# Performance work log

Measured on AMD Instinct MI355X. Metric: run time of the kernel, lower is better.

The kernel has to match this reference:

```python
import jax, jax.numpy as jnp
import numpy as np

BATCH, HID, STEPS = 64, 2048, 30

def setup_inputs() -> dict:
    key = jax.random.key(0)
    ks = jax.random.split(key, 7)
    s = 1.0 / np.sqrt(HID)  # pytorch LSTM/Linear init scale
    return {
        "monthly_token": jax.random.normal(ks[0], (BATCH, HID), jnp.float32),
        "steps": STEPS,
        "W_ih": jax.random.uniform(ks[1], (4 * HID, HID), jnp.float32, -s, s),
        "W_hh": jax.random.uniform(ks[2], (4 * HID, HID), jnp.float32, -s, s),
        "b_ih": jax.random.uniform(ks[3], (4 * HID,), jnp.float32, -s, s),
        "b_hh": jax.random.uniform(ks[4], (4 * HID,), jnp.float32, -s, s),
        "W_out": jax.random.uniform(ks[5], (1, HID), jnp.float32, -s, s),
        "b_out": jax.random.uniform(ks[6], (1,), jnp.float32, -s, s),
    }

def reference(monthly_token, steps, W_ih, W_hh, b_ih, b_hh, W_out, b_out):
    H = monthly_token.shape[1]
    h0 = monthly_token                      # (B, H) initial hidden
    c0 = jnp.zeros_like(h0)
    x0 = jnp.zeros_like(h0)                 # first lstm input is zeros

    def step(carry, _):
        h, c, x = carry
        # PyTorch gate order: input, forget, cell(g), output
        gates = x @ W_ih.T + b_ih + h @ W_hh.T + b_hh   # (B, 4H)
        i, f, g, o = jnp.split(gates, 4, axis=-1)
        i = jax.nn.sigmoid(i)
        f = jax.nn.sigmoid(f)
        g = jnp.tanh(g)
        o = jax.nn.sigmoid(o)
        c_new = f * c + i * g
        h_new = o * jnp.tanh(c_new)
        y = h_new @ W_out.T + b_out          # (B, 1) daily value
        # feedback: next input is the lstm output (= h_new for 1-layer LSTM)
        return (h_new, c_new, h_new), y[:, 0]

    _, ys = jax.lax.scan(step, (h0, c0, x0), xs=None, length=steps)
    return ys.T                               # (B, steps)
```

## Files before the change

kernel.cpp:

```cpp
#include <hip/hip_runtime.h>
#include <cmath>


#define HID   2048
#define BATCH 64
#define G4    8192
#define NCU   256
#define HGRP  (HID * BATCH / 8)
#define NFLAGS 512

typedef __attribute__((ext_vector_type(8))) _Float16 half8;
typedef __attribute__((ext_vector_type(4))) float f32x4;

#define LDS_BYTES 155648

__global__ void k_init(const float* __restrict__ token, const float* __restrict__ bih,
                       const float* __restrict__ bhh, half8* __restrict__ h0p,
                       float* __restrict__ bsum, unsigned* __restrict__ flags) {
    int g = blockIdx.x * 256 + threadIdx.x;
    int l = g & 63, nt = (g >> 6) & 3, kt = g >> 8;
    int n = nt * 16 + (l & 15);
    int k0 = kt * 32 + (l >> 4) * 8;
    const float4* ps = (const float4*)(token + (size_t)n * HID + k0);
    float4 a = ps[0], b = ps[1];
    half8 v;
    v[0]=(_Float16)a.x; v[1]=(_Float16)a.y; v[2]=(_Float16)a.z; v[3]=(_Float16)a.w;
    v[4]=(_Float16)b.x; v[5]=(_Float16)b.y; v[6]=(_Float16)b.z; v[7]=(_Float16)b.w;
    h0p[g] = v;
    if (g < G4) bsum[g] = bih[g] + bhh[g];
    if (g < NFLAGS) flags[g] = 0u;
}

__global__ __launch_bounds__(512, 2)
void k_lstm(const float* __restrict__ wih, const float* __restrict__ whh,
            const float* __restrict__ bsum, const float* __restrict__ wout,
            _Float16* __restrict__ hbuf,
            float* __restrict__ ypart,
            unsigned* __restrict__ flags, int steps) {
    extern __shared__ char smem[];
    half8* Wlds = (half8*)smem;
    f32x4* red4 = (f32x4*)(smem + 131072);

    const int tid  = threadIdx.x;
    const int blk  = blockIdx.x;
    const int lane = tid & 63;
    const int w    = tid >> 6;
    const int half = w & 1;
    const int ks   = w >> 1;
    const int q    = lane >> 4;
    const int col  = lane & 15;

    for (int idx = tid; idx < 2 * 64 * 64; idx += 512) {
        int l = idx & 63, kt = (idx >> 6) & 63, m2 = idx >> 12;
        int m = l & 15;
        int gate = m2 * 2 + (m >> 3);
        int row  = gate * HID + blk * 8 + (m & 7);
        int colw = kt * 32 + (l >> 4) * 8;
        const float4* p = (const float4*)(whh + (size_t)row * HID + colw);
        float4 a = p[0], b = p[1];
        half8 v;
        v[0]=(_Float16)a.x; v[1]=(_Float16)a.y; v[2]=(_Float16)a.z; v[3]=(_Float16)a.w;
        v[4]=(_Float16)b.x; v[5]=(_Float16)b.y; v[6]=(_Float16)b.z; v[7]=(_Float16)b.w;
        Wlds[idx] = v;
    }

    float biasA[4] = {0,0,0,0}, biasB[4] = {0,0,0,0}, wj4[4] = {0,0,0,0};
    float c4[4] = {0.0f, 0.0f, 0.0f, 0.0f};
    if (w < 2) {
        #pragma unroll
        for (int r = 0; r < 4; ++r) {
            int rA = 4 * q + r;
            int rB = 16 + 4 * q + r;
            biasA[r] = bsum[(rA >> 3) * HID + blk * 8 + (rA & 7)];
            biasB[r] = bsum[(rB >> 3) * HID + blk * 8 + (rB & 7)];
            wj4[r]   = wout[blk * 8 + (q & 1) * 4 + r];
        }
    }
    __syncthreads();

    for (int t = 0; t < steps; ++t) {
        if (t) {
            while (__hip_atomic_load(&flags[half * NCU + ks * 64 + lane],
                                     __ATOMIC_RELAXED, __HIP_MEMORY_SCOPE_AGENT)
                   < (unsigned)t)
                __builtin_amdgcn_s_sleep(1);
            asm volatile("" ::: "memory");
        }
        const half8* hp = (const half8*)(hbuf + (size_t)t * HID * BATCH);
        const int ktb = ks * 16;
        half8 bfr[32];
        #pragma unroll
        for (int kk = 0; kk < 16; ++kk) {
            bfr[2 * kk + 0] = hp[((ktb + kk) * 4 + half * 2 + 0) * 64 + lane];
            bfr[2 * kk + 1] = hp[((ktb + kk) * 4 + half * 2 + 1) * 64 + lane];
        }
        f32x4 a00 = {0,0,0,0}, a01 = {0,0,0,0}, a10 = {0,0,0,0}, a11 = {0,0,0,0};
        #pragma unroll
        for (int kk = 0; kk < 16; ++kk) {
            int kt = ktb + kk;
            half8 av0 = Wlds[(kt) * 64 + lane];
            half8 av1 = Wlds[(64 + kt) * 64 + lane];
            a00 = __builtin_amdgcn_mfma_f32_16x16x32_f16(av0, bfr[2 * kk + 0], a00, 0, 0, 0);
            a01 = __builtin_amdgcn_mfma_f32_16x16x32_f16(av0, bfr[2 * kk + 1], a01, 0, 0, 0);
            a10 = __builtin_amdgcn_mfma_f32_16x16x32_f16(av1, bfr[2 * kk + 0], a10, 0, 0, 0);
            a11 = __builtin_amdgcn_mfma_f32_16x16x32_f16(av1, bfr[2 * kk + 1], a11, 0, 0, 0);
        }
        if (ks == 1 || ks == 3) {
            int srow = (ks == 3 ? 2 : 0) + half;
            red4[(srow * 4 + 0) * 64 + lane] = a00;
            red4[(srow * 4 + 1) * 64 + lane] = a01;
            red4[(srow * 4 + 2) * 64 + lane] = a10;
            red4[(srow * 4 + 3) * 64 + lane] = a11;
        }
        __syncthreads();
        if (ks == 0) {
            int srow = half;
            a00 += red4[(srow * 4 + 0) * 64 + lane];
            a01 += red4[(srow * 4 + 1) * 64 + lane];
            a10 += red4[(srow * 4 + 2) * 64 + lane];
            a11 += red4[(srow * 4 + 3) * 64 + lane];
        } else if (ks == 2) {
            int srow = 2 + half;
            a00 += red4[(srow * 4 + 0) * 64 + lane];
            a01 += red4[(srow * 4 + 1) * 64 + lane];
            a10 += red4[(srow * 4 + 2) * 64 + lane];
            a11 += red4[(srow * 4 + 3) * 64 + lane];
            int sdst = 4 + half;
            red4[(sdst * 4 + 0) * 64 + lane] = a00;
            red4[(sdst * 4 + 1) * 64 + lane] = a01;
            red4[(sdst * 4 + 2) * 64 + lane] = a10;
            red4[(sdst * 4 + 3) * 64 + lane] = a11;
        }
        __syncthreads();
        if (w < 2) {
            int srow = 4 + half;
            a00 += red4[(srow * 4 + 0) * 64 + lane];
            a01 += red4[(srow * 4 + 1) * 64 + lane];
            a10 += red4[(srow * 4 + 2) * 64 + lane];
            a11 += red4[(srow * 4 + 3) * 64 + lane];
            #pragma unroll
            for (int r = 0; r < 4; ++r) {
                a00[r] += biasA[r]; a01[r] += biasA[r];
                a10[r] += biasB[r]; a11[r] += biasB[r];
            }
            float x00[4], x01[4], x10[4], x11[4];
            #pragma unroll
            for (int r = 0; r < 4; ++r) {
                x00[r] = __shfl_xor(a00[r], 32);
                x01[r] = __shfl_xor(a01[r], 32);
                x10[r] = __shfl_xor(a10[r], 32);
                x11[r] = __shfl_xor(a11[r], 32);
            }
            const bool lo = (lane < 32);
            float hv[4];
            #pragma unroll
            for (int r = 0; r < 4; ++r) {
                float gi = lo ? a00[r] : x01[r];
                float gf = lo ? x00[r] : a01[r];
                float gg = lo ? a10[r] : x11[r];
                float go = lo ? x10[r] : a11[r];
                float iv = 1.0f / (1.0f + __expf(-gi));
                float fv = 1.0f / (1.0f + __expf(-gf));
                float eg = __expf(2.0f * gg);
                float gv = 1.0f - 2.0f / (eg + 1.0f);
                float ov = 1.0f / (1.0f + __expf(-go));
                c4[r] = fv * c4[r] + iv * gv;
                float ec = __expf(2.0f * c4[r]);
                float th = 1.0f - 2.0f / (ec + 1.0f);
                hv[r] = ov * th;
            }
            if (t < steps - 1) {
                union { unsigned short us[4]; unsigned long long ull; } pk;
                #pragma unroll
                for (int r = 0; r < 4; ++r) {
                    _Float16 hf = (_Float16)hv[r];
                    pk.us[r] = *(unsigned short*)&hf;
                }
                const int nt = half * 2 + (q >> 1);
                const size_t g = (size_t)((blk >> 2) * 4 + nt) * 64
                               + (blk & 3) * 16 + col;
                unsigned long long* dst = (unsigned long long*)
                    (hbuf + (size_t)(t + 1) * HID * BATCH + g * 8) + (q & 1);
                __hip_atomic_store(dst, pk.ull, __ATOMIC_RELAXED,
                                   __HIP_MEMORY_SCOPE_AGENT);
                asm volatile("s_waitcnt vmcnt(0)" ::: "memory");
                if (lane == 0)
                    __hip_atomic_store(&flags[half * NCU + blk], (unsigned)(t + 1),
                                       __ATOMIC_RELAXED, __HIP_MEMORY_SCOPE_AGENT);
            }
            float yp = wj4[0] * hv[0] + wj4[1] * hv[1]
                     + wj4[2] * hv[2] + wj4[3] * hv[3];
            yp += __shfl_xor(yp, 16);
            if ((q & 1) == 0)
                ypart[((size_t)t * NCU + blk) * 64
                      + half * 32 + (q >> 1) * 16 + col] = yp;
        }
        if (t == 0) {
            for (int idx = tid; idx < 2 * 64 * 64; idx += 512) {
                int l = idx & 63, kt = (idx >> 6) & 63, m2 = idx >> 12;
                int m = l & 15;
                int gate = m2 * 2 + (m >> 3);
                int row  = gate * HID + blk * 8 + (m & 7);
                int colw = kt * 32 + (l >> 4) * 8;
                const float4* p = (const float4*)(wih + (size_t)row * HID + colw);
                float4 a = p[0], b = p[1];
                half8 v = Wlds[idx];
                v[0] = (_Float16)((float)v[0] + a.x); v[1] = (_Float16)((float)v[1] + a.y);
                v[2] = (_Float16)((float)v[2] + a.z); v[3] = (_Float16)((float)v[3] + a.w);
                v[4] = (_Float16)((float)v[4] + b.x); v[5] = (_Float16)((float)v[5] + b.y);
                v[6] = (_Float16)((float)v[6] + b.z); v[7] = (_Float16)((float)v[7] + b.w);
                Wlds[idx] = v;
            }
            __syncthreads();
        }
    }
}

__global__ __launch_bounds__(512)
void k_yout(const float* __restrict__ ypart, const float* __restrict__ bout,
            float* __restrict__ out, int steps) {
    __shared__ float red[8][64];
    int t = blockIdx.x;
    int tid = threadIdx.x;
    int b = tid & 63, ch = tid >> 6;
    const float* p = ypart + (size_t)t * NCU * 64 + b;
    float s = 0.0f;
    #pragma unroll 8
    for (int cu = ch * 32; cu < ch * 32 + 32; ++cu) s += p[(size_t)cu * 64];
    red[ch][b] = s;
    __syncthreads();
    if (tid < 64) {
        float r = bout[0];
        #pragma unroll
        for (int u = 0; u < 8; ++u) r += red[u][tid];
        out[(size_t)tid * steps + t] = r;
    }
}

extern "C" void kernel_launch(void* const* d_in, const int* in_sizes, int n_in,
                              void* d_out, int out_size, void* d_ws, size_t ws_size,
                              hipStream_t stream) {
    const float* token = (const float*)d_in[0];
    const float* wih   = (const float*)d_in[2];
    const float* whh   = (const float*)d_in[3];
    const float* bih   = (const float*)d_in[4];
    const float* bhh   = (const float*)d_in[5];
    const float* wout  = (const float*)d_in[6];
    const float* bout  = (const float*)d_in[7];
    float* out = (float*)d_out;
    const int steps = out_size / BATCH;

    char* ws = (char*)d_ws;
    size_t off = 0;
    auto carve = [&](size_t bytes) -> void* {
        void* p = ws + off;
        off = (off + bytes + 255) & ~(size_t)255;
        return p;
    };
    _Float16* hbuf  = (_Float16*)carve((size_t)(steps + 1) * HID * BATCH * 2);
    float*    bsum  = (float*)carve((size_t)G4 * 4);
    float*    ypart = (float*)carve((size_t)steps * NCU * 64 * 4);
    unsigned* flags = (unsigned*)carve(NFLAGS * 4);

    hipFuncSetAttribute(reinterpret_cast<const void*>(&k_lstm),
                        hipFuncAttributeMaxDynamicSharedMemorySize, LDS_BYTES);

    k_init<<<dim3(HGRP / 256), dim3(256), 0, stream>>>(
        token, bih, bhh, (half8*)hbuf, bsum, flags);

    k_lstm<<<dim3(NCU), dim3(512), LDS_BYTES, stream>>>(
        wih, whh, bsum, wout, hbuf, ypart, flags, steps);

    k_yout<<<dim3(steps), dim3(512), 0, stream>>>(ypart, bout, out, steps);
}
```

Baseline: 440.6 us.

## Replace per-step flag barrier with sentinel-valued hidden-state polling

```diff
diff --git a/kernel.cpp b/kernel.cpp
--- a/kernel.cpp
+++ b/kernel.cpp
@@ -7,7 +7,7 @@
 #define G4    8192
 #define NCU   256
 #define HGRP  (HID * BATCH / 8)
-#define NFLAGS 512
+#define SENT  0xFFFFFFFFFFFFFFFFull
 
 typedef __attribute__((ext_vector_type(8))) _Float16 half8;
 typedef __attribute__((ext_vector_type(4))) float f32x4;
@@ -15,20 +15,26 @@
 #define LDS_BYTES 155648
 
 __global__ void k_init(const float* __restrict__ token, const float* __restrict__ bih,
-                       const float* __restrict__ bhh, half8* __restrict__ h0p,
-                       float* __restrict__ bsum, unsigned* __restrict__ flags) {
-    int g = blockIdx.x * 256 + threadIdx.x;
-    int l = g & 63, nt = (g >> 6) & 3, kt = g >> 8;
-    int n = nt * 16 + (l & 15);
-    int k0 = kt * 32 + (l >> 4) * 8;
-    const float4* ps = (const float4*)(token + (size_t)n * HID + k0);
-    float4 a = ps[0], b = ps[1];
-    half8 v;
-    v[0]=(_Float16)a.x; v[1]=(_Float16)a.y; v[2]=(_Float16)a.z; v[3]=(_Float16)a.w;
-    v[4]=(_Float16)b.x; v[5]=(_Float16)b.y; v[6]=(_Float16)b.z; v[7]=(_Float16)b.w;
-    h0p[g] = v;
-    if (g < G4) bsum[g] = bih[g] + bhh[g];
-    if (g < NFLAGS) flags[g] = 0u;
+                       const float* __restrict__ bhh, half8* __restrict__ hbuf8,
+                       float* __restrict__ bsum) {
+    int slot = blockIdx.x >> 6;
+    int g = (blockIdx.x & 63) * 256 + threadIdx.x;
+    if (slot == 0) {
+        int l = g & 63, nt = (g >> 6) & 3, kt = g >> 8;
+        int n = nt * 16 + (l & 15);
+        int k0 = kt * 32 + (l >> 4) * 8;
+        const float4* ps = (const float4*)(token + (size_t)n * HID + k0);
+        float4 a = ps[0], b = ps[1];
+        half8 v;
+        v[0]=(_Float16)a.x; v[1]=(_Float16)a.y; v[2]=(_Float16)a.z; v[3]=(_Float16)a.w;
+        v[4]=(_Float16)b.x; v[5]=(_Float16)b.y; v[6]=(_Float16)b.z; v[7]=(_Float16)b.w;
+        hbuf8[g] = v;
+        if (g < G4) bsum[g] = bih[g] + bhh[g];
+    } else {
+        unsigned long long* d =
+            (unsigned long long*)(hbuf8 + (size_t)slot * HGRP + g);
+        d[0] = SENT; d[1] = SENT;
+    }
 }
 
 __global__ __launch_bounds__(512, 2)
@@ -36,7 +42,7 @@
             const float* __restrict__ bsum, const float* __restrict__ wout,
             _Float16* __restrict__ hbuf,
             float* __restrict__ ypart,
-            unsigned* __restrict__ flags, int steps) {
+            int steps) {
     extern __shared__ char smem[];
     half8* Wlds = (half8*)smem;
     f32x4* red4 = (f32x4*)(smem + 131072);
@@ -79,20 +85,31 @@
     __syncthreads();
 
     for (int t = 0; t < steps; ++t) {
-        if (t) {
-            while (__hip_atomic_load(&flags[half * NCU + ks * 64 + lane],
-                                     __ATOMIC_RELAXED, __HIP_MEMORY_SCOPE_AGENT)
-                   < (unsigned)t)
-                __builtin_amdgcn_s_sleep(1);
-            asm volatile("" ::: "memory");
-        }
-        const half8* hp = (const half8*)(hbuf + (size_t)t * HID * BATCH);
+        const _Float16* hslot = hbuf + (size_t)t * HID * BATCH;
         const int ktb = ks * 16;
-        half8 bfr[32];
-        #pragma unroll
-        for (int kk = 0; kk < 16; ++kk) {
-            bfr[2 * kk + 0] = hp[((ktb + kk) * 4 + half * 2 + 0) * 64 + lane];
-            bfr[2 * kk + 1] = hp[((ktb + kk) * 4 + half * 2 + 1) * 64 + lane];
+        unsigned long long b64[64];
+        #pragma unroll
+        for (int p = 0; p < 32; ++p) {
+            int kk = p >> 1, j = p & 1;
+            const unsigned long long* wp = (const unsigned long long*)
+                (hslot + (size_t)(((ktb + kk) * 4 + half * 2 + j) * 64 + lane) * 8);
+            b64[2 * p + 0] = __hip_atomic_load(wp, __ATOMIC_RELAXED,
+                                               __HIP_MEMORY_SCOPE_AGENT);
+            b64[2 * p + 1] = __hip_atomic_load(wp + 1, __ATOMIC_RELAXED,
+                                               __HIP_MEMORY_SCOPE_AGENT);
+        }
+        __builtin_amdgcn_sched_barrier(0);
+        #pragma unroll
+        for (int p = 0; p < 32; ++p) {
+            int kk = p >> 1, j = p & 1;
+            const unsigned long long* wp = (const unsigned long long*)
+                (hslot + (size_t)(((ktb + kk) * 4 + half * 2 + j) * 64 + lane) * 8);
+            while (!__all((b64[2 * p] != SENT) && (b64[2 * p + 1] != SENT))) {
+                b64[2 * p + 0] = __hip_atomic_load(wp, __ATOMIC_RELAXED,
+                                                   __HIP_MEMORY_SCOPE_AGENT);
+                b64[2 * p + 1] = __hip_atomic_load(wp + 1, __ATOMIC_RELAXED,
+                                                   __HIP_MEMORY_SCOPE_AGENT);
+            }
         }
         f32x4 a00 = {0,0,0,0}, a01 = {0,0,0,0}, a10 = {0,0,0,0}, a11 = {0,0,0,0};
         #pragma unroll
@@ -100,10 +117,13 @@
             int kt = ktb + kk;
             half8 av0 = Wlds[(kt) * 64 + lane];
             half8 av1 = Wlds[(64 + kt) * 64 + lane];
-            a00 = __builtin_amdgcn_mfma_f32_16x16x32_f16(av0, bfr[2 * kk + 0], a00, 0, 0, 0);
-            a01 = __builtin_amdgcn_mfma_f32_16x16x32_f16(av0, bfr[2 * kk + 1], a01, 0, 0, 0);
-            a10 = __builtin_amdgcn_mfma_f32_16x16x32_f16(av1, bfr[2 * kk + 0], a10, 0, 0, 0);
-            a11 = __builtin_amdgcn_mfma_f32_16x16x32_f16(av1, bfr[2 * kk + 1], a11, 0, 0, 0);
+            union { unsigned long long u[2]; half8 h; } c0, c1;
+            c0.u[0] = b64[4 * kk + 0]; c0.u[1] = b64[4 * kk + 1];
+            c1.u[0] = b64[4 * kk + 2]; c1.u[1] = b64[4 * kk + 3];
+            a00 = __builtin_amdgcn_mfma_f32_16x16x32_f16(av0, c0.h, a00, 0, 0, 0);
+            a01 = __builtin_amdgcn_mfma_f32_16x16x32_f16(av0, c1.h, a01, 0, 0, 0);
+            a10 = __builtin_amdgcn_mfma_f32_16x16x32_f16(av1, c0.h, a10, 0, 0, 0);
+            a11 = __builtin_amdgcn_mfma_f32_16x16x32_f16(av1, c1.h, a11, 0, 0, 0);
         }
         if (ks == 1 || ks == 3) {
             int srow = (ks == 3 ? 2 : 0) + half;
@@ -183,10 +203,6 @@
                     (hbuf + (size_t)(t + 1) * HID * BATCH + g * 8) + (q & 1);
                 __hip_atomic_store(dst, pk.ull, __ATOMIC_RELAXED,
                                    __HIP_MEMORY_SCOPE_AGENT);
-                asm volatile("s_waitcnt vmcnt(0)" ::: "memory");
-                if (lane == 0)
-                    __hip_atomic_store(&flags[half * NCU + blk], (unsigned)(t + 1),
-                                       __ATOMIC_RELAXED, __HIP_MEMORY_SCOPE_AGENT);
             }
             float yp = wj4[0] * hv[0] + wj4[1] * hv[1]
                      + wj4[2] * hv[2] + wj4[3] * hv[3];
@@ -260,16 +276,15 @@
     _Float16* hbuf  = (_Float16*)carve((size_t)(steps + 1) * HID * BATCH * 2);
     float*    bsum  = (float*)carve((size_t)G4 * 4);
     float*    ypart = (float*)carve((size_t)steps * NCU * 64 * 4);
-    unsigned* flags = (unsigned*)carve(NFLAGS * 4);
 
     hipFuncSetAttribute(reinterpret_cast<const void*>(&k_lstm),
                         hipFuncAttributeMaxDynamicSharedMemorySize, LDS_BYTES);
 
-    k_init<<<dim3(HGRP / 256), dim3(256), 0, stream>>>(
-        token, bih, bhh, (half8*)hbuf, bsum, flags);
+    k_init<<<dim3(64 * steps), dim3(256), 0, stream>>>(
+        token, bih, bhh, (half8*)hbuf, bsum);
 
     k_lstm<<<dim3(NCU), dim3(512), LDS_BYTES, stream>>>(
-        wih, whh, bsum, wout, hbuf, ypart, flags, steps);
+        wih, whh, bsum, wout, hbuf, ypart, steps);
 
     k_yout<<<dim3(steps), dim3(512), 0, stream>>>(ypart, bout, out, steps);
 }
```

Result: slower. 574.3 us (+30.4%).
